# Performance work log

Hardware: AMD Instinct MI355X
Metric: run time of the kernel (lower is better)

## Reference

```python
import jax, jax.numpy as jnp
import numpy as np

N_NODES = 100000
N_EDGES = 800000
D = 96
BN_EPS = 1e-5
LEAKY_SLOPE = 0.05


def setup_inputs() -> dict:
    key = jax.random.key(0)
    ks = jax.random.split(key, 6)
    node_feat = jax.random.normal(ks[0], (N_NODES, D), dtype=jnp.float32)
    edge_index = jax.random.randint(ks[1], (2, N_EDGES), 0, N_NODES, dtype=jnp.int64)
    W1 = jax.random.normal(ks[2], (D, D), dtype=jnp.float32) / np.sqrt(D)
    b1 = jnp.zeros((D,), dtype=jnp.float32)
    W2 = jax.random.normal(ks[3], (D, D), dtype=jnp.float32) / np.sqrt(D)
    b2 = jnp.zeros((D,), dtype=jnp.float32)
    bn_gamma = jnp.ones((D,), dtype=jnp.float32)
    bn_beta = jnp.zeros((D,), dtype=jnp.float32)
    bn_mean = jnp.zeros((D,), dtype=jnp.float32)
    bn_var = jax.random.uniform(ks[4], (D,), dtype=jnp.float32, minval=0.5, maxval=1.5)
    return {"node_feat": node_feat, "edge_index": edge_index, "W1": W1, "b1": b1,
            "W2": W2, "b2": b2, "bn_gamma": bn_gamma, "bn_beta": bn_beta,
            "bn_mean": bn_mean, "bn_var": bn_var}


def _gcn_norm(edge_index, n_nodes, dtype):
    # add self-loops, symmetric normalization D^{-1/2} (A+I) D^{-1/2}
    loop = jnp.arange(n_nodes, dtype=edge_index.dtype)
    src = jnp.concatenate([edge_index[0], loop])
    dst = jnp.concatenate([edge_index[1], loop])
    deg = jax.ops.segment_sum(jnp.ones(src.shape, dtype=dtype), dst, num_segments=n_nodes)
    dinv = jnp.where(deg > 0, jax.lax.rsqrt(jnp.maximum(deg, 1e-12)), 0.0)
    norm = dinv[src] * dinv[dst]  # [E+N]
    return src, dst, norm


def _gcn_conv(x, W, b, src, dst, norm, n_nodes):
    h = x @ W                              # [N, d_out] dense GEMM
    msg = h[src] * norm[:, None]           # gather + scale, [E+N, d_out]
    agg = jax.ops.segment_sum(msg, dst, num_segments=n_nodes)  # scatter-add
    return agg + b


def reference(node_feat, edge_index, W1, b1, W2, b2, bn_gamma, bn_beta, bn_mean, bn_var):
    n = node_feat.shape[0]
    src, dst, norm = _gcn_norm(edge_index, n, node_feat.dtype)
    # layer 1: GCNConv -> LeakyReLU(0.05) -> BatchNorm1d (eval) -> dropout(eval = identity)
    x = _gcn_conv(node_feat, W1, b1, src, dst, norm, n)
    x = jnp.where(x >= 0, x, LEAKY_SLOPE * x)
    x = (x - bn_mean) * jax.lax.rsqrt(bn_var + BN_EPS) * bn_gamma + bn_beta
    # layer 2 (final): GCNConv only
    x = _gcn_conv(x, W2, b2, src, dst, norm, n)
    return x
```

## Files before the change

### kernel.cpp

```cpp
#include <hip/hip_runtime.h>

#define DF 96
#define BN_EPS 1e-5f
#define SLOPE 0.05f
#define LPN 12
#define GBLK 192
#define NPBG (GBLK / LPN)

typedef __attribute__((ext_vector_type(8))) short bf16x8;
typedef __attribute__((ext_vector_type(4))) float f32x4;
typedef __attribute__((ext_vector_type(4))) unsigned short u16x4;
typedef __attribute__((ext_vector_type(8))) unsigned short u16x8;

__device__ __forceinline__ unsigned short f2bf(float f) {
    unsigned u = __builtin_bit_cast(unsigned, f);
    return (unsigned short)((u + 0x7FFFu + ((u >> 16) & 1u)) >> 16);
}
__device__ __forceinline__ float bf2f(unsigned short h) {
    return __builtin_bit_cast(float, (unsigned)h << 16);
}

__global__ __launch_bounds__(256) void k_prep(const float* __restrict__ gamma,
                                              const float* __restrict__ beta,
                                              const float* __restrict__ mean,
                                              const float* __restrict__ var,
                                              float* __restrict__ bnscale,
                                              float* __restrict__ bnbias,
                                              const float* __restrict__ W1,
                                              const float* __restrict__ W2,
                                              unsigned short* __restrict__ Wt1,
                                              unsigned short* __restrict__ Wt2,
                                              int* __restrict__ cnt, int n) {
    int i = blockIdx.x * 256 + threadIdx.x;
    if (i < DF * DF) {
        int nn = i / DF, k = i - nn * DF;
        Wt1[i] = f2bf(W1[k * DF + nn]);
        Wt2[i] = f2bf(W2[k * DF + nn]);
    }
    if (i < DF) {
        float s = gamma[i] * rsqrtf(var[i] + BN_EPS);
        bnscale[i] = s;
        bnbias[i]  = beta[i] - mean[i] * s;
    }
    if (i < n) cnt[i] = 0;
}

__global__ __launch_bounds__(256) void k_countrank(const int* __restrict__ ei,
                                                   int* __restrict__ cnt,
                                                   int* __restrict__ rank, int E) {
    int e = blockIdx.x * 256 + threadIdx.x;
    if (e < E) rank[e] = atomicAdd(&cnt[ei[E + e]], 1);
}

__global__ __launch_bounds__(256) void k_scan1(const int* __restrict__ cnt,
                                               int* __restrict__ rowptr,
                                               int* __restrict__ bsum, int n) {
    __shared__ int sh[256];
    int t = threadIdx.x;
    int i = blockIdx.x * 256 + t;
    int x = (i < n) ? cnt[i] : 0;
    sh[t] = x;
    __syncthreads();
#pragma unroll
    for (int off = 1; off < 256; off <<= 1) {
        int v = (t >= off) ? sh[t - off] : 0;
        __syncthreads();
        sh[t] += v;
        __syncthreads();
    }
    if (i < n) rowptr[i] = sh[t] - x;
    if (t == 255) bsum[blockIdx.x] = sh[255];
}

__global__ __launch_bounds__(512) void k_scan23(int* __restrict__ rowptr,
                                                const int* __restrict__ bsum,
                                                const int* __restrict__ cnt,
                                                float* __restrict__ dinv,
                                                int n, int E, int nb) {
    __shared__ int sh[512];
    __shared__ int sbex[512];
    const int t = threadIdx.x;
    int x = (t < nb) ? bsum[t] : 0;
    sh[t] = x;
    __syncthreads();
#pragma unroll
    for (int off = 1; off < 512; off <<= 1) {
        int v = (t >= off) ? sh[t - off] : 0;
        __syncthreads();
        sh[t] += v;
        __syncthreads();
    }
    sbex[t] = sh[t] - x;
    __syncthreads();

    const int i = blockIdx.x * 512 + t;
    if (i < n) {
        rowptr[i] = rowptr[i] + sbex[i >> 8];
        dinv[i]   = rsqrtf((float)cnt[i] + 1.0f);
    }
    if (i == 0) rowptr[n] = E;
}

__global__ __launch_bounds__(256) void k_fill(const int* __restrict__ ei,
                                              const int* __restrict__ rowptr,
                                              const int* __restrict__ rank,
                                              int* __restrict__ csr, int E) {
    int e = blockIdx.x * 256 + threadIdx.x;
    if (e < E) {
        int src = ei[e];
        int dst = ei[E + e];
        csr[rowptr[dst] + rank[e]] = src;
    }
}

template <int LAYER>
__global__ __launch_bounds__(256) void k_gemm(const void* __restrict__ in_,
                                              const unsigned short* __restrict__ Wt,
                                              const float* __restrict__ dinv,
                                              unsigned short* __restrict__ outb, int n) {
    const int tid  = threadIdx.x;
    const int wave = tid >> 6;
    const int lane = tid & 63;
    const int l16  = lane & 15;
    const int quad = lane >> 4;
    const int rowbase = blockIdx.x * 64 + wave * 16;
    const int m = rowbase + l16;
    const bool valid = (m < n);

    bf16x8 bfrag[6][3];
#pragma unroll
    for (int nt = 0; nt < 6; ++nt)
#pragma unroll
        for (int ks = 0; ks < 3; ++ks)
            bfrag[nt][ks] = *(const bf16x8*)&Wt[(nt * 16 + l16) * DF + ks * 32 + quad * 8];

    bf16x8 afrag[3];
    const bf16x8 zf = {};
    if (LAYER == 0) {
        const float* in = (const float*)in_;
        const float* rowp = in + (size_t)m * DF;
        float4 ra[3][2];
#pragma unroll
        for (int ks = 0; ks < 3; ++ks) {
            if (valid) {
                ra[ks][0] = *(const float4*)&rowp[ks * 32 + quad * 8];
                ra[ks][1] = *(const float4*)&rowp[ks * 32 + quad * 8 + 4];
            } else {
                ra[ks][0] = make_float4(0.f, 0.f, 0.f, 0.f);
                ra[ks][1] = make_float4(0.f, 0.f, 0.f, 0.f);
            }
        }
#pragma unroll
        for (int ks = 0; ks < 3; ++ks) {
            const float* a0 = (const float*)&ra[ks][0];
            const float* a1 = (const float*)&ra[ks][1];
            bf16x8 f;
#pragma unroll
            for (int j = 0; j < 4; ++j) {
                f[j]     = (short)f2bf(a0[j]);
                f[j + 4] = (short)f2bf(a1[j]);
            }
            afrag[ks] = f;
        }
    } else {
        const unsigned short* in = (const unsigned short*)in_;
#pragma unroll
        for (int ks = 0; ks < 3; ++ks)
            afrag[ks] = valid ? *(const bf16x8*)&in[(size_t)m * DF + ks * 32 + quad * 8] : zf;
    }

    f32x4 acc[6] = {};
#pragma unroll
    for (int ks = 0; ks < 3; ++ks)
#pragma unroll
        for (int nt = 0; nt < 6; ++nt)
            acc[nt] = __builtin_amdgcn_mfma_f32_16x16x32_bf16(afrag[ks], bfrag[nt][ks],
                                                              acc[nt], 0, 0, 0);

#pragma unroll
    for (int reg = 0; reg < 4; ++reg) {
        const int r = rowbase + quad * 4 + reg;
        if (r < n) {
            const float dv = dinv[r];
#pragma unroll
            for (int nt = 0; nt < 6; ++nt)
                outb[(size_t)r * DF + nt * 16 + l16] = f2bf(acc[nt][reg] * dv);
        }
    }
}

template <int LAYER>
__global__ __launch_bounds__(GBLK) void k_gather(const int* __restrict__ rowptr,
                                                 const int* __restrict__ csr,
                                                 const unsigned short* __restrict__ hs,
                                                 const float* __restrict__ dinv,
                                                 const float* __restrict__ b1,
                                                 const float* __restrict__ bnscale,
                                                 const float* __restrict__ bnbias,
                                                 const float* __restrict__ b2,
                                                 void* __restrict__ outp, int n) {
    const int t = threadIdx.x;
    const int v = blockIdx.x * NPBG + t / LPN;
    const int q = t % LPN;
    if (v >= n) return;

    float acc[8];
    {
        const u16x8 h0 = *(const u16x8*)&hs[(size_t)v * DF + q * 8];
#pragma unroll
        for (int i = 0; i < 8; ++i) acc[i] = bf2f(h0[i]);
    }

    const int e0 = rowptr[v];
    const int e1 = rowptr[v + 1];
    int e = e0;
    for (; e + 8 <= e1; e += 8) {
        int s[8];
#pragma unroll
        for (int u = 0; u < 8; ++u) s[u] = csr[e + u];
        u16x8 m[8];
#pragma unroll
        for (int u = 0; u < 8; ++u) m[u] = *(const u16x8*)&hs[(size_t)s[u] * DF + q * 8];
#pragma unroll
        for (int u = 0; u < 8; ++u)
#pragma unroll
            for (int i = 0; i < 8; ++i) acc[i] += bf2f(m[u][i]);
    }
    for (; e + 4 <= e1; e += 4) {
        int s[4];
#pragma unroll
        for (int u = 0; u < 4; ++u) s[u] = csr[e + u];
        u16x8 m[4];
#pragma unroll
        for (int u = 0; u < 4; ++u) m[u] = *(const u16x8*)&hs[(size_t)s[u] * DF + q * 8];
#pragma unroll
        for (int u = 0; u < 4; ++u)
#pragma unroll
            for (int i = 0; i < 8; ++i) acc[i] += bf2f(m[u][i]);
    }
    for (; e < e1; ++e) {
        const int s = csr[e];
        const u16x8 m = *(const u16x8*)&hs[(size_t)s * DF + q * 8];
#pragma unroll
        for (int i = 0; i < 8; ++i) acc[i] += bf2f(m[i]);
    }

    const float dv = dinv[v];
    if (LAYER == 0) {
        u16x8 o;
#pragma unroll
        for (int i = 0; i < 8; ++i) {
            const int c = q * 8 + i;
            float x = __builtin_fmaf(dv, acc[i], b1[c]);
            x = (x >= 0.f) ? x : SLOPE * x;
            o[i] = f2bf(__builtin_fmaf(x, bnscale[c], bnbias[c]));
        }
        *(u16x8*)((unsigned short*)outp + (size_t)v * DF + q * 8) = o;
    } else {
        float* op = (float*)outp + (size_t)v * DF + q * 8;
        float4 o0, o1;
        o0.x = __builtin_fmaf(acc[0], dv, b2[q * 8 + 0]);
        o0.y = __builtin_fmaf(acc[1], dv, b2[q * 8 + 1]);
        o0.z = __builtin_fmaf(acc[2], dv, b2[q * 8 + 2]);
        o0.w = __builtin_fmaf(acc[3], dv, b2[q * 8 + 3]);
        o1.x = __builtin_fmaf(acc[4], dv, b2[q * 8 + 4]);
        o1.y = __builtin_fmaf(acc[5], dv, b2[q * 8 + 5]);
        o1.z = __builtin_fmaf(acc[6], dv, b2[q * 8 + 6]);
        o1.w = __builtin_fmaf(acc[7], dv, b2[q * 8 + 7]);
        *(float4*)op       = o0;
        *(float4*)(op + 4) = o1;
    }
}

extern "C" void kernel_launch(void* const* d_in, const int* in_sizes, int n_in,
                              void* d_out, int out_size, void* d_ws, size_t ws_size,
                              hipStream_t stream) {
    const float* node_feat = (const float*)d_in[0];
    const int*   ei        = (const int*)d_in[1];
    const float* W1        = (const float*)d_in[2];
    const float* b1        = (const float*)d_in[3];
    const float* W2        = (const float*)d_in[4];
    const float* b2        = (const float*)d_in[5];
    const float* gamma     = (const float*)d_in[6];
    const float* beta      = (const float*)d_in[7];
    const float* mean      = (const float*)d_in[8];
    const float* var       = (const float*)d_in[9];

    const int n  = in_sizes[0] / DF;
    const int E  = in_sizes[1] / 2;
    const int nb = (n + 255) / 256;

    char* base = (char*)d_ws;
    size_t off = 0;
    auto alloc = [&](size_t bytes) { void* p = base + off; off = (off + bytes + 15) & ~(size_t)15; return p; };
    int*   cnt     = (int*)alloc(sizeof(int) * n);
    int*   rowptr  = (int*)alloc(sizeof(int) * (n + 1));
    int*   bsum    = (int*)alloc(sizeof(int) * 512);
    float* dinv    = (float*)alloc(sizeof(float) * n);
    float* bnscale = (float*)alloc(sizeof(float) * DF);
    float* bnbias  = (float*)alloc(sizeof(float) * DF);
    unsigned short* Wt1 = (unsigned short*)alloc(sizeof(short) * DF * DF);
    unsigned short* Wt2 = (unsigned short*)alloc(sizeof(short) * DF * DF);
    int*   rank    = (int*)alloc(sizeof(int) * E);
    int*   csr     = (int*)alloc(sizeof(int) * E);
    unsigned short* bufA = (unsigned short*)alloc(sizeof(short) * (size_t)n * DF);
    unsigned short* bufB = (unsigned short*)alloc(sizeof(short) * (size_t)n * DF);
    float* out     = (float*)d_out;

    k_prep<<<nb, 256, 0, stream>>>(gamma, beta, mean, var, bnscale, bnbias,
                                   W1, W2, Wt1, Wt2, cnt, n);
    k_countrank<<<(E + 255) / 256, 256, 0, stream>>>(ei, cnt, rank, E);
    k_scan1<<<nb, 256, 0, stream>>>(cnt, rowptr, bsum, n);
    k_scan23<<<(n + 511) / 512, 512, 0, stream>>>(rowptr, bsum, cnt, dinv, n, E, nb);
    k_fill<<<(E + 255) / 256, 256, 0, stream>>>(ei, rowptr, rank, csr, E);

    const int gblocks  = (n + 63) / 64;
    const int gagather = (n + NPBG - 1) / NPBG;

    k_gemm<0><<<gblocks, 256, 0, stream>>>(node_feat, Wt1, dinv, bufA, n);
    k_gather<0><<<gagather, GBLK, 0, stream>>>(rowptr, csr, bufA, dinv, b1, bnscale,
                                               bnbias, b2, bufB, n);
    k_gemm<1><<<gblocks, 256, 0, stream>>>(bufB, Wt2, dinv, bufA, n);
    k_gather<1><<<gagather, GBLK, 0, stream>>>(rowptr, csr, bufA, dinv, b1, bnscale,
                                               bnbias, b2, out, n);
}
```

Measured before the change: 265.5 us.

## Merge CSR fill into layer-1 GEMM launch and pair edges in countrank

The CSR fill kernel becomes extra blocks of the layer-1 GEMM launch. Since the GEMM only depends on dinv, the scatter-fill can run alongside it, and one kernel launch and its drain bubble go away. Separately, countrank now handles two edges per thread using vectorized int2 loads and stores. The risks are uneven block mixing in the fused launch and slightly different atomic contention patterns.

```diff
diff --git a/kernel.cpp b/kernel.cpp
--- a/kernel.cpp
+++ b/kernel.cpp
@@ -9,7 +9,6 @@
 
 typedef __attribute__((ext_vector_type(8))) short bf16x8;
 typedef __attribute__((ext_vector_type(4))) float f32x4;
-typedef __attribute__((ext_vector_type(4))) unsigned short u16x4;
 typedef __attribute__((ext_vector_type(8))) unsigned short u16x8;
 
 __device__ __forceinline__ unsigned short f2bf(float f) {
@@ -48,8 +47,16 @@
 __global__ __launch_bounds__(256) void k_countrank(const int* __restrict__ ei,
                                                    int* __restrict__ cnt,
                                                    int* __restrict__ rank, int E) {
-    int e = blockIdx.x * 256 + threadIdx.x;
-    if (e < E) rank[e] = atomicAdd(&cnt[ei[E + e]], 1);
+    int i = blockIdx.x * 256 + threadIdx.x;
+    int e = i * 2;
+    if (e + 1 < E) {
+        int2 d = *(const int2*)&ei[E + e];
+        int r0 = atomicAdd(&cnt[d.x], 1);
+        int r1 = atomicAdd(&cnt[d.y], 1);
+        *(int2*)&rank[e] = make_int2(r0, r1);
+    } else if (e < E) {
+        rank[e] = atomicAdd(&cnt[ei[E + e]], 1);
+    }
 }
 
 __global__ __launch_bounds__(256) void k_scan1(const int* __restrict__ cnt,
@@ -101,29 +108,16 @@
     if (i == 0) rowptr[n] = E;
 }
 
-__global__ __launch_bounds__(256) void k_fill(const int* __restrict__ ei,
-                                              const int* __restrict__ rowptr,
-                                              const int* __restrict__ rank,
-                                              int* __restrict__ csr, int E) {
-    int e = blockIdx.x * 256 + threadIdx.x;
-    if (e < E) {
-        int src = ei[e];
-        int dst = ei[E + e];
-        csr[rowptr[dst] + rank[e]] = src;
-    }
-}
-
 template <int LAYER>
-__global__ __launch_bounds__(256) void k_gemm(const void* __restrict__ in_,
-                                              const unsigned short* __restrict__ Wt,
-                                              const float* __restrict__ dinv,
-                                              unsigned short* __restrict__ outb, int n) {
-    const int tid  = threadIdx.x;
+__device__ __forceinline__ void gemm_body(int bid, int tid, const void* __restrict__ in_,
+                                          const unsigned short* __restrict__ Wt,
+                                          const float* __restrict__ dinv,
+                                          unsigned short* __restrict__ outb, int n) {
     const int wave = tid >> 6;
     const int lane = tid & 63;
     const int l16  = lane & 15;
     const int quad = lane >> 4;
-    const int rowbase = blockIdx.x * 64 + wave * 16;
+    const int rowbase = bid * 64 + wave * 16;
     const int m = rowbase + l16;
     const bool valid = (m < n);
 
@@ -187,6 +181,39 @@
                 outb[(size_t)r * DF + nt * 16 + l16] = f2bf(acc[nt][reg] * dv);
         }
     }
+}
+
+__device__ __forceinline__ void fill_body(int bid, int tid, const int* __restrict__ ei,
+                                          const int* __restrict__ rowptr,
+                                          const int* __restrict__ rank,
+                                          int* __restrict__ csr, int E) {
+    int e = bid * 256 + tid;
+    if (e < E) {
+        int src = ei[e];
+        int dst = ei[E + e];
+        csr[rowptr[dst] + rank[e]] = src;
+    }
+}
+
+__global__ __launch_bounds__(256) void k_gemm1_fill(const float* __restrict__ in,
+                                                    const unsigned short* __restrict__ Wt1,
+                                                    const float* __restrict__ dinv,
+                                                    unsigned short* __restrict__ bufA,
+                                                    int n, int gb,
+                                                    const int* __restrict__ ei,
+                                                    const int* __restrict__ rowptr,
+                                                    const int* __restrict__ rank,
+                                                    int* __restrict__ csr, int E) {
+    const int b = blockIdx.x;
+    if (b < gb) gemm_body<0>(b, threadIdx.x, in, Wt1, dinv, bufA, n);
+    else        fill_body(b - gb, threadIdx.x, ei, rowptr, rank, csr, E);
+}
+
+__global__ __launch_bounds__(256) void k_gemm2(const unsigned short* __restrict__ in,
+                                               const unsigned short* __restrict__ Wt2,
+                                               const float* __restrict__ dinv,
+                                               unsigned short* __restrict__ outb, int n) {
+    gemm_body<1>(blockIdx.x, threadIdx.x, in, Wt2, dinv, outb, n);
 }
 
 template <int LAYER>
@@ -309,18 +336,19 @@
 
     k_prep<<<nb, 256, 0, stream>>>(gamma, beta, mean, var, bnscale, bnbias,
                                    W1, W2, Wt1, Wt2, cnt, n);
-    k_countrank<<<(E + 255) / 256, 256, 0, stream>>>(ei, cnt, rank, E);
+    k_countrank<<<(E / 2 + 255) / 256, 256, 0, stream>>>(ei, cnt, rank, E);
     k_scan1<<<nb, 256, 0, stream>>>(cnt, rowptr, bsum, n);
     k_scan23<<<(n + 511) / 512, 512, 0, stream>>>(rowptr, bsum, cnt, dinv, n, E, nb);
-    k_fill<<<(E + 255) / 256, 256, 0, stream>>>(ei, rowptr, rank, csr, E);
-
-    const int gblocks  = (n + 63) / 64;
+
+    const int gb = (n + 63) / 64;
+    const int fb = (E + 255) / 256;
     const int gagather = (n + NPBG - 1) / NPBG;
 
-    k_gemm<0><<<gblocks, 256, 0, stream>>>(node_feat, Wt1, dinv, bufA, n);
+    k_gemm1_fill<<<gb + fb, 256, 0, stream>>>(node_feat, Wt1, dinv, bufA, n, gb,
+                                              ei, rowptr, rank, csr, E);
     k_gather<0><<<gagather, GBLK, 0, stream>>>(rowptr, csr, bufA, dinv, b1, bnscale,
                                                bnbias, b2, bufB, n);
-    k_gemm<1><<<gblocks, 256, 0, stream>>>(bufB, Wt2, dinv, bufA, n);
+    k_gemm2<<<gb, 256, 0, stream>>>(bufB, Wt2, dinv, bufA, n);
     k_gather<1><<<gagather, GBLK, 0, stream>>>(rowptr, csr, bufA, dinv, b1, bnscale,
                                                bnbias, b2, out, n);
 }
```

After: 261.7 us. No clear change (-1.4%).
